# Performance work log

Measured on AMD Instinct MI355X. Metric: run time of the kernel, lower is better.

## Reference

```python
import jax, jax.numpy as jnp
import numpy as np

V, N, D, H, C = 3, 4096, 512, 128, 5  # views, nodes, in_dim, hidden, classes
NEG = -9.0e15   # mask value from original code (-9000000000000000.0)
NEG_SLOPE = 0.25


def _leaky(x, slope):
    return jnp.where(x >= 0, x, slope * x)


def setup_inputs() -> dict:
    key = jax.random.key(0)
    ks = jax.random.split(key, 24)
    g = lambda i, shape, s=0.05: (jax.random.normal(ks[i], shape, dtype=jnp.float32) * s)
    return {
        "data": jax.random.normal(ks[0], (V, N, D), dtype=jnp.float32),
        "adj": jax.random.randint(ks[1], (V, N, N), 0, 2, dtype=jnp.int32),
        "gac_w": g(2, (V, D, H)), "gac_b": g(3, (V, H)),
        "a1": g(4, (V, H)), "a2": g(5, (V, H)),
        "mlp_w": g(6, (V, D, H)), "mlp_b": g(7, (V, H)),
        "q_w": g(8, (V, H, H)), "q_b": g(9, (V, H)),
        "k_w": g(10, (V, H, H)), "k_b": g(11, (V, H)),
        "v_w": g(12, (V, H, H)), "v_b": g(13, (V, H)),
        "fc_w": g(14, (V, H, H)), "fc_b": g(15, (V, H)),
        "conf_w": g(16, (V, H, 1)), "conf_b": g(17, (V, 1)),
        "mm_w": g(18, (V * H, C)), "mm_b": g(19, (C,)),
    }


def reference(data, adj, gac_w, gac_b, a1, a2, mlp_w, mlp_b,
              q_w, q_b, k_w, k_b, v_w, v_b, fc_w, fc_b,
              conf_w, conf_b, mm_w, mm_b):
    # --- GraphAttentionConv (per view, vectorized over v) ---
    h = jnp.einsum('vnd,vdh->vnh', data, gac_w)               # spmm(input, W)
    e1 = jnp.einsum('vnh,vh->vn', h, a1)                      # h @ a1
    e2 = jnp.einsum('vnh,vh->vn', h, a2)                      # h @ a2
    e = _leaky(e1[:, :, None] + e2[:, None, :], NEG_SLOPE)    # [V,N,N] broadcast-add
    e = jnp.where(adj > 0, e, NEG)                            # mask by dense adjacency
    att = jax.nn.softmax(e, axis=-1)                          # row softmax
    feat = jnp.einsum('vnm,vmh->vnh', att, h) + gac_b[:, None, :]
    feat = _leaky(feat, NEG_SLOPE)                            # F.leaky_relu(GAC out, 0.25)
    # residual MLP branch
    feat = feat + jnp.einsum('vnd,vdh->vnh', data, mlp_w) + mlp_b[:, None, :]

    # --- StructureGuidedFeatureEnhancement (n_heads=1): per-node HxH attention ---
    Q = jnp.einsum('vnh,vho->vno', feat, q_w) + q_b[:, None, :]
    K = jnp.einsum('vnh,vho->vno', feat, k_w) + k_b[:, None, :]
    Vv = jnp.einsum('vnh,vho->vno', feat, v_w) + v_b[:, None, :]
    scale = jnp.sqrt(jnp.asarray(H, jnp.float32))
    A = Q[:, :, :, None] * K[:, :, None, :] / scale           # [V,N,H,H] outer product
    A = jax.nn.softmax(A, axis=-1)
    agg = jnp.einsum('vnio,vno->vni', A, Vv)                  # attention @ V
    agg = jnp.einsum('vnh,vho->vno', agg, fc_w) + fc_b[:, None, :]
    feat = jax.nn.relu(agg)

    # --- TCP confidence gating ---
    conf = jnp.einsum('vnh,vho->vno', feat, conf_w) + conf_b[:, None, :]  # [V,N,1]
    feat = feat * conf

    # --- concat views along feature dim, final classifier ---
    mm = jnp.transpose(feat, (1, 0, 2)).reshape(N, V * H)     # [N, V*H]
    return mm @ mm_w + mm_b                                   # MMlogit [N, C]
```

## Files before the change

kernel.cpp:

```cpp
#include <hip/hip_runtime.h>
#include <hip/hip_bf16.h>

#define V 3
#define N 4096
#define D 512
#define H 128
#define C 5
#define KS 2
#define LOG2E 1.4426950408889634f

typedef short short8 __attribute__((ext_vector_type(8)));
typedef float floatx4 __attribute__((ext_vector_type(4)));
typedef int   intx4  __attribute__((ext_vector_type(4)));

__device__ __forceinline__ unsigned short f2bf(float f){
  __hip_bfloat16 h = __float2bfloat16(f);
  return *reinterpret_cast<unsigned short*>(&h);
}
__device__ __forceinline__ unsigned int pk_bf16(float a, float b){
  unsigned int ua = __float_as_uint(a), ub = __float_as_uint(b);
  ua += 0x7FFFu + ((ua >> 16) & 1u);
  ub += 0x7FFFu + ((ub >> 16) & 1u);
  return (ua >> 16) | (ub & 0xFFFF0000u);
}

#define TN1 16
__global__ __launch_bounds__(256) void k1_gemm(
    const float* __restrict__ data,
    const float* __restrict__ gac_w,
    const float* __restrict__ mlp_w,
    const float* __restrict__ a1, const float* __restrict__ a2,
    unsigned short* __restrict__ hT, float* __restrict__ mlp_out,
    float* __restrict__ e1, float* __restrict__ e2)
{
  const int v = blockIdx.y;
  const int n0 = blockIdx.x * TN1;
  const int t = threadIdx.x;
  const int half = t >> 7, tt = t & 127;
  __shared__ float ds[D][20];
  __shared__ float epart[2][2][TN1];
  float* comb = &ds[0][0];
  const float* dp = data + ((size_t)v*N + n0)*D;
  for (int j = t; j < TN1*D; j += 256){
    int r = j >> 9, d = j & (D-1);
    ds[d][r] = dp[(size_t)r*D + d];
  }
  __syncthreads();
  float ag[TN1], am[TN1];
  #pragma unroll
  for (int r=0;r<TN1;r++){ ag[r]=0.f; am[r]=0.f; }
  const int d0 = half*256;
  const float* gw = gac_w + (size_t)v*D*H + tt;
  const float* mw = mlp_w + (size_t)v*D*H + tt;
  for (int d=d0; d<d0+256; d++){
    float wg = gw[(size_t)d*H];
    float wm = mw[(size_t)d*H];
    const float4* p = (const float4*)&ds[d][0];
    float4 x0=p[0], x1=p[1], x2=p[2], x3=p[3];
    float xv[16] = {x0.x,x0.y,x0.z,x0.w, x1.x,x1.y,x1.z,x1.w,
                    x2.x,x2.y,x2.z,x2.w, x3.x,x3.y,x3.z,x3.w};
    #pragma unroll
    for (int r=0;r<TN1;r++){
      ag[r] = fmaf(xv[r], wg, ag[r]);
      am[r] = fmaf(xv[r], wm, am[r]);
    }
  }
  __syncthreads();
  if (half == 1){
    #pragma unroll
    for (int r=0;r<TN1;r++){
      comb[r*H + tt]          = ag[r];
      comb[TN1*H + r*H + tt]  = am[r];
    }
  }
  __syncthreads();
  if (half == 0){
    float* mp = mlp_out + ((size_t)v*N + n0)*H + tt;
    unsigned short pk[TN1];
    const float a1v = a1[v*H + tt], a2v = a2[v*H + tt];
    #pragma unroll
    for (int r=0;r<TN1;r++){
      ag[r] += comb[r*H + tt];
      am[r] += comb[TN1*H + r*H + tt];
      mp[(size_t)r*H] = am[r];
      pk[r] = f2bf(ag[r]);
    }
    uint4* hp = (uint4*)(hT + ((size_t)v*H + tt)*N + n0);
    hp[0] = *(uint4*)&pk[0];
    hp[1] = *(uint4*)&pk[8];
    #pragma unroll
    for (int r=0;r<TN1;r++){
      float s1 = ag[r]*a1v, s2 = ag[r]*a2v;
      #pragma unroll
      for (int o=32;o>0;o>>=1){ s1 += __shfl_down(s1,o); s2 += __shfl_down(s2,o); }
      if ((tt&63)==0){ epart[0][tt>>6][r]=s1; epart[1][tt>>6][r]=s2; }
    }
  }
  __syncthreads();
  if (t < TN1)        e1[(size_t)v*N + n0 + t]       = LOG2E*(epart[0][0][t]    + epart[0][1][t]);
  else if (t < 2*TN1) e2[(size_t)v*N + n0 + (t-TN1)] = LOG2E*(epart[1][0][t-TN1]+ epart[1][1][t-TN1]);
}

#define KC2 256
__global__ __launch_bounds__(512, 8) void k2_attn(
    const unsigned short* __restrict__ hT, const int* __restrict__ adj,
    const float* __restrict__ e1g, const float* __restrict__ e2g,
    float* __restrict__ pacc, float* __restrict__ pdenG)
{
  const int v = blockIdx.z;
  const int ksid = blockIdx.y;
  const int n0 = blockIdx.x * 16;
  const int kbase = ksid * (N/KS);
  const int t = threadIdx.x;
  const int w = t >> 6, flane = t & 63;
  const int row = flane & 15, quad = flane >> 4;
  __shared__ __align__(16) unsigned short Afrag[2][8][64][8];
  __shared__ float pden_l[8][16];

  const intx4* ap4 = (const intx4*)(adj + ((size_t)v*N + n0 + row)*N
                                    + kbase + w*32 + quad*8);
  const float4* ep4 = (const float4*)(e2g + (size_t)v*N + kbase + w*32 + quad*8);
  const float e1r = e1g[(size_t)v*N + n0 + row];
  float psum = 0.f;

  const int col = w*16 + row;
  const unsigned short* bcol = hT + ((size_t)v*H + col)*N + kbase + quad*8;
  floatx4 acc = {0.f, 0.f, 0.f, 0.f};

  intx4  av0 = __builtin_nontemporal_load(ap4);
  intx4  av1 = __builtin_nontemporal_load(ap4 + 1);
  float4 ev0 = ep4[0];
  float4 ev1 = ep4[1];

  const int NCH = (N/KS)/KC2;
  #pragma unroll 1
  for (int c = 0; c < NCH; c++){
    {
      float ev[8] = {ev0.x,ev0.y,ev0.z,ev0.w, ev1.x,ev1.y,ev1.z,ev1.w};
      int   aa[8] = {av0.x,av0.y,av0.z,av0.w, av1.x,av1.y,av1.z,av1.w};
      float wv[8];
      #pragma unroll
      for (int j=0;j<8;j++){
        float y = e1r + ev[j];
        y = fmaxf(y, 0.25f*y);
        float e = exp2f(y);
        wv[j] = (aa[j] > 0) ? e : 0.f;
        psum += wv[j];
      }
      union { short8 s; unsigned int u[4]; } a8;
      #pragma unroll
      for (int j=0;j<4;j++) a8.u[j] = pk_bf16(wv[2*j], wv[2*j+1]);
      *(short8*)&Afrag[c&1][w][flane][0] = a8.s;
    }
    if (c+1 < NCH){
      av0 = __builtin_nontemporal_load(ap4 + (c+1)*64);
      av1 = __builtin_nontemporal_load(ap4 + (c+1)*64 + 1);
      ev0 = ep4[(c+1)*64];
      ev1 = ep4[(c+1)*64 + 1];
    }
    __syncthreads();
    const int m0 = c * KC2;
    #pragma unroll
    for (int ks=0; ks<8; ks++){
      short8 a8 = *(const short8*)&Afrag[c&1][ks][flane][0];
      short8 b8 = *(const short8*)(bcol + m0 + ks*32);
      acc = __builtin_amdgcn_mfma_f32_16x16x32_bf16(a8, b8, acc, 0, 0, 0);
    }
    __syncthreads();
  }
  psum += __shfl_down(psum, 32);
  psum += __shfl_down(psum, 16);
  if (flane < 16) pden_l[w][flane] = psum;
  __syncthreads();
  const size_t pb = (((size_t)v*KS + ksid)*(N/16) + blockIdx.x);
  float* pa = pacc + pb*(16*H);
  #pragma unroll
  for (int reg=0; reg<4; reg++){
    const int r = quad*4 + reg;
    pa[r*H + col] = acc[reg];
  }
  if (t < 16){
    float den = 0.f;
    #pragma unroll
    for (int k=0;k<8;k++) den += pden_l[k][t];
    pdenG[pb*16 + t] = den;
  }
}

__global__ __launch_bounds__(256) void k2_reduce(
    const float* __restrict__ pacc, const float* __restrict__ pdenG,
    const float* __restrict__ mlp_out,
    const float* __restrict__ gac_b, const float* __restrict__ mlp_b,
    float* __restrict__ feat)
{
  const int v = blockIdx.y;
  const int n0 = blockIdx.x * 16;
  const int t = threadIdx.x;
  const int col = t & 127, rh = t >> 7;
  const size_t pb0 = (((size_t)v*KS + 0)*(N/16) + blockIdx.x);
  const size_t pb1 = (((size_t)v*KS + 1)*(N/16) + blockIdx.x);
  const float* pa0 = pacc + pb0*(16*H);
  const float* pa1 = pacc + pb1*(16*H);
  const float gb = gac_b[v*H + col];
  const float mb = mlp_b[v*H + col];
  #pragma unroll
  for (int i=0;i<8;i++){
    const int r = rh*8 + i;
    float num = pa0[r*H + col] + pa1[r*H + col];
    float den = pdenG[pb0*16 + r] + pdenG[pb1*16 + r];
    float x = num/den + gb;
    x = (x >= 0.f) ? x : 0.25f*x;
    const size_t idx = ((size_t)v*N + n0 + r)*H + col;
    feat[idx] = x + mlp_out[idx] + mb;
  }
}

#define TN3 8
__global__ __launch_bounds__(128) void k3_sgfe(
    const float* __restrict__ feat,
    const float* __restrict__ qw, const float* __restrict__ qb,
    const float* __restrict__ kw, const float* __restrict__ kb,
    const float* __restrict__ vw, const float* __restrict__ vb,
    const float* __restrict__ fcw, const float* __restrict__ fcb,
    const float* __restrict__ confw, const float* __restrict__ confb,
    float* __restrict__ feat2)
{
  const int v = blockIdx.y;
  const int n0 = blockIdx.x * TN3;
  const int t = threadIdx.x;
  const int W = t >> 6, lane = t & 63;
  __shared__ float fsT[H][12];
  __shared__ float Qs[TN3][H];
  __shared__ float2 KVs[TN3][H];
  __shared__ float As2T[H][12];
  __shared__ float rbuf2[TN3][2];
  const float* fp = feat + ((size_t)v*N + n0)*H + t;
  #pragma unroll
  for (int r=0;r<TN3;r++) fsT[t][r] = fp[(size_t)r*H];
  __syncthreads();
  const float* qwp = qw + (size_t)v*H*H + t;
  const float* kwp = kw + (size_t)v*H*H + t;
  const float* vwp = vw + (size_t)v*H*H + t;
  float Qr[TN3], Kr[TN3], Vr[TN3];
  {
    const float qbv = qb[v*H+t], kbv = kb[v*H+t], vbv = vb[v*H+t];
    #pragma unroll
    for (int r=0;r<TN3;r++){ Qr[r]=qbv; Kr[r]=kbv; Vr[r]=vbv; }
  }
  for (int i=0;i<H;i++){
    float wq = qwp[(size_t)i*H];
    float wk = kwp[(size_t)i*H];
    float wv = vwp[(size_t)i*H];
    float4 f0 = *(const float4*)&fsT[i][0];
    float4 f1 = *(const float4*)&fsT[i][4];
    float fv[8] = {f0.x,f0.y,f0.z,f0.w, f1.x,f1.y,f1.z,f1.w};
    #pragma unroll
    for (int r=0;r<TN3;r++){
      Qr[r] = fmaf(fv[r], wq, Qr[r]);
      Kr[r] = fmaf(fv[r], wk, Kr[r]);
      Vr[r] = fmaf(fv[r], wv, Vr[r]);
    }
  }
  #pragma unroll
  for (int r=0;r<TN3;r++){
    Qs[r][t] = Qr[r];
    KVs[r][t] = make_float2(Kr[r], Vr[r]);
  }
  __syncthreads();
  const float invs = 0.08838834764831845f;
  #pragma unroll
  for (int p=0;p<4;p++){
    const int r = 2*p + W;
    const float qa = Qs[r][lane]   * invs;
    const float qb2 = Qs[r][lane+64] * invs;
    float sA=0.f, aA=0.f, sB=0.f, aB=0.f;
    const float4* kvp = (const float4*)&KVs[r][0];
    #pragma unroll 4
    for (int oo=0; oo<H/2; oo++){
      float4 kv2 = kvp[oo];
      float eA0 = __expf(qa*kv2.x);  sA += eA0; aA = fmaf(eA0, kv2.y, aA);
      float eA1 = __expf(qa*kv2.z);  sA += eA1; aA = fmaf(eA1, kv2.w, aA);
      float eB0 = __expf(qb2*kv2.x); sB += eB0; aB = fmaf(eB0, kv2.y, aB);
      float eB1 = __expf(qb2*kv2.z); sB += eB1; aB = fmaf(eB1, kv2.w, aB);
    }
    As2T[lane][r]    = aA/sA;
    As2T[lane+64][r] = aB/sB;
  }
  __syncthreads();
  const float* fcwp = fcw + (size_t)v*H*H + t;
  const float fcbv = fcb[v*H+t];
  float g[TN3];
  #pragma unroll
  for (int r=0;r<TN3;r++) g[r] = fcbv;
  for (int i=0;i<H;i++){
    float fw = fcwp[(size_t)i*H];
    float4 a0 = *(const float4*)&As2T[i][0];
    float4 a1v = *(const float4*)&As2T[i][4];
    g[0] = fmaf(a0.x, fw, g[0]);  g[1] = fmaf(a0.y, fw, g[1]);
    g[2] = fmaf(a0.z, fw, g[2]);  g[3] = fmaf(a0.w, fw, g[3]);
    g[4] = fmaf(a1v.x, fw, g[4]); g[5] = fmaf(a1v.y, fw, g[5]);
    g[6] = fmaf(a1v.z, fw, g[6]); g[7] = fmaf(a1v.w, fw, g[7]);
  }
  const float cwv = confw[v*H+t];
  const float cbv = confb[v];
  #pragma unroll
  for (int r=0;r<TN3;r++){
    g[r] = fmaxf(g[r], 0.f);
    float psm = g[r]*cwv;
    #pragma unroll
    for (int o=32;o>0;o>>=1) psm += __shfl_down(psm,o);
    if (lane==0) rbuf2[r][W] = psm;
  }
  __syncthreads();
  #pragma unroll
  for (int r=0;r<TN3;r++){
    const float conf = rbuf2[r][0] + rbuf2[r][1] + cbv;
    feat2[((size_t)v*N + n0 + r)*H + t] = g[r]*conf;
  }
}

__global__ __launch_bounds__(64) void k4_cls(
    const float* __restrict__ feat2,
    const float* __restrict__ mm_w, const float* __restrict__ mm_b,
    float* __restrict__ out)
{
  const int n = blockIdx.x, t = threadIdx.x;
  float a[C] = {0,0,0,0,0};
  for (int j=t; j<V*H; j+=64){
    int vv = j >> 7, hh = j & (H-1);
    float f = feat2[((size_t)vv*N + n)*H + hh];
    #pragma unroll
    for (int c=0;c<C;c++) a[c] = fmaf(f, mm_w[j*C+c], a[c]);
  }
  #pragma unroll
  for (int c=0;c<C;c++){
    #pragma unroll
    for (int o=32;o>0;o>>=1) a[c] += __shfl_down(a[c],o);
  }
  if (t==0){
    #pragma unroll
    for (int c=0;c<C;c++) out[(size_t)n*C+c] = a[c] + mm_b[c];
  }
}

extern "C" void kernel_launch(void* const* d_in, const int* in_sizes, int n_in,
                              void* d_out, int out_size, void* d_ws, size_t ws_size,
                              hipStream_t stream)
{
  (void)in_sizes; (void)n_in; (void)out_size; (void)ws_size;
  const float* data  = (const float*)d_in[0];
  const int*   adj   = (const int*)d_in[1];
  const float* gac_w = (const float*)d_in[2];
  const float* gac_b = (const float*)d_in[3];
  const float* a1    = (const float*)d_in[4];
  const float* a2    = (const float*)d_in[5];
  const float* mlp_w = (const float*)d_in[6];
  const float* mlp_b = (const float*)d_in[7];
  const float* q_w   = (const float*)d_in[8];
  const float* q_b   = (const float*)d_in[9];
  const float* k_w   = (const float*)d_in[10];
  const float* k_b   = (const float*)d_in[11];
  const float* v_w   = (const float*)d_in[12];
  const float* v_b   = (const float*)d_in[13];
  const float* fc_w  = (const float*)d_in[14];
  const float* fc_b  = (const float*)d_in[15];
  const float* cw    = (const float*)d_in[16];
  const float* cb    = (const float*)d_in[17];
  const float* mm_w  = (const float*)d_in[18];
  const float* mm_b  = (const float*)d_in[19];

  float* ws = (float*)d_ws;
  const size_t VNH = (size_t)V*N*H;
  float* mlp   = ws;
  float* feat  = ws + VNH;
  float* feat2 = ws + 2*VNH;
  float* e1    = ws + 3*VNH;
  float* e2    = e1 + (size_t)V*N;
  unsigned short* hT = (unsigned short*)(e2 + (size_t)V*N);
  float* pacc  = (float*)(hT + VNH);
  float* pden  = pacc + (size_t)V*KS*(N/16)*16*H;

  k1_gemm<<<dim3(N/TN1, V), 256, 0, stream>>>(data, gac_w, mlp_w, a1, a2,
                                              hT, mlp, e1, e2);
  k2_attn<<<dim3(N/16, KS, V), 512, 0, stream>>>(hT, adj, e1, e2, pacc, pden);
  k2_reduce<<<dim3(N/16, V), 256, 0, stream>>>(pacc, pden, mlp, gac_b, mlp_b, feat);
  k3_sgfe<<<dim3(N/TN3, V), 128, 0, stream>>>(feat, q_w, q_b, k_w, k_b, v_w, v_b,
                                              fc_w, fc_b, cw, cb, feat2);
  k4_cls<<<dim3(N),          64, 0, stream>>>(feat2, mm_w, mm_b, (float*)d_out);
}
```

Before: 525.1 us.

## Widen attention tile to 64 rows and split K four ways for hT reuse

The masked-softmax attention kernel now processes 64 query rows per block, with four row tiles sharing each hT B-fragment load across four MFMAs. Each wave handles two rows and one K-slice. The K dimension is split into 4 partitions instead of 2, and the reduce kernel is widened to sum four partials over 64-row tiles. This cuts repeated global reads of the bf16 hidden features, which were previously reloaded for every 16-row tile. In exchange it uses more registers and LDS per block and writes more partial-sum traffic to global memory.

```diff
diff --git a/kernel.cpp b/kernel.cpp
--- a/kernel.cpp
+++ b/kernel.cpp
@@ -6,7 +6,8 @@
 #define D 512
 #define H 128
 #define C 5
-#define KS 2
+#define KS 4
+#define M2 64
 #define LOG2E 1.4426950408889634f
 
 typedef short short8 __attribute__((ext_vector_type(8)));
@@ -101,116 +102,149 @@
   else if (t < 2*TN1) e2[(size_t)v*N + n0 + (t-TN1)] = LOG2E*(epart[1][0][t-TN1]+ epart[1][1][t-TN1]);
 }
 
-#define KC2 256
-__global__ __launch_bounds__(512, 8) void k2_attn(
+__global__ __launch_bounds__(512, 4) void k2_attn(
     const unsigned short* __restrict__ hT, const int* __restrict__ adj,
     const float* __restrict__ e1g, const float* __restrict__ e2g,
     float* __restrict__ pacc, float* __restrict__ pdenG)
 {
   const int v = blockIdx.z;
   const int ksid = blockIdx.y;
-  const int n0 = blockIdx.x * 16;
+  const int n0 = blockIdx.x * M2;
   const int kbase = ksid * (N/KS);
   const int t = threadIdx.x;
-  const int w = t >> 6, flane = t & 63;
-  const int row = flane & 15, quad = flane >> 4;
-  __shared__ __align__(16) unsigned short Afrag[2][8][64][8];
-  __shared__ float pden_l[8][16];
-
-  const intx4* ap4 = (const intx4*)(adj + ((size_t)v*N + n0 + row)*N
-                                    + kbase + w*32 + quad*8);
-  const float4* ep4 = (const float4*)(e2g + (size_t)v*N + kbase + w*32 + quad*8);
-  const float e1r = e1g[(size_t)v*N + n0 + row];
-  float psum = 0.f;
-
-  const int col = w*16 + row;
+  const int w = t >> 6, l = t & 63;
+  __shared__ __align__(16) unsigned short Afrag[2][4][4][64][8];
+  __shared__ float pden_sh[M2][4];
+
+  const int ksl  = w & 3;
+  const int quad = l >> 4;
+  const int rt0  = w >> 2;
+  const int row0 = rt0*16 + (l & 15);
+  const int row1 = row0 + 32;
+  const int koff = ksl*32 + quad*8;
+  const intx4* ap0 = (const intx4*)(adj + ((size_t)v*N + n0 + row0)*N + kbase + koff);
+  const intx4* ap1 = (const intx4*)(adj + ((size_t)v*N + n0 + row1)*N + kbase + koff);
+  const float4* ep = (const float4*)(e2g + (size_t)v*N + kbase + koff);
+  const float e1r0 = e1g[(size_t)v*N + n0 + row0];
+  const float e1r1 = e1g[(size_t)v*N + n0 + row1];
+  float psum0 = 0.f, psum1 = 0.f;
+
+  const int col = w*16 + (l & 15);
   const unsigned short* bcol = hT + ((size_t)v*H + col)*N + kbase + quad*8;
-  floatx4 acc = {0.f, 0.f, 0.f, 0.f};
-
-  intx4  av0 = __builtin_nontemporal_load(ap4);
-  intx4  av1 = __builtin_nontemporal_load(ap4 + 1);
-  float4 ev0 = ep4[0];
-  float4 ev1 = ep4[1];
-
-  const int NCH = (N/KS)/KC2;
+  floatx4 acc[4];
+  #pragma unroll
+  for (int rt=0;rt<4;rt++) acc[rt] = (floatx4){0.f,0.f,0.f,0.f};
+
+  intx4  a00 = __builtin_nontemporal_load(ap0);
+  intx4  a01 = __builtin_nontemporal_load(ap0 + 1);
+  intx4  a10 = __builtin_nontemporal_load(ap1);
+  intx4  a11 = __builtin_nontemporal_load(ap1 + 1);
+  float4 ev0 = ep[0];
+  float4 ev1 = ep[1];
+
+  const int NCH = (N/KS)/128;
   #pragma unroll 1
   for (int c = 0; c < NCH; c++){
+    const int buf = c & 1;
     {
       float ev[8] = {ev0.x,ev0.y,ev0.z,ev0.w, ev1.x,ev1.y,ev1.z,ev1.w};
-      int   aa[8] = {av0.x,av0.y,av0.z,av0.w, av1.x,av1.y,av1.z,av1.w};
-      float wv[8];
+      int   aa[8] = {a00.x,a00.y,a00.z,a00.w, a01.x,a01.y,a01.z,a01.w};
+      int   bb[8] = {a10.x,a10.y,a10.z,a10.w, a11.x,a11.y,a11.z,a11.w};
+      float wa[8], wb[8];
       #pragma unroll
       for (int j=0;j<8;j++){
-        float y = e1r + ev[j];
-        y = fmaxf(y, 0.25f*y);
-        float e = exp2f(y);
-        wv[j] = (aa[j] > 0) ? e : 0.f;
-        psum += wv[j];
+        float ya = e1r0 + ev[j];
+        ya = fmaxf(ya, 0.25f*ya);
+        float ea = exp2f(ya);
+        wa[j] = (aa[j] > 0) ? ea : 0.f;
+        psum0 += wa[j];
+        float yb = e1r1 + ev[j];
+        yb = fmaxf(yb, 0.25f*yb);
+        float eb = exp2f(yb);
+        wb[j] = (bb[j] > 0) ? eb : 0.f;
+        psum1 += wb[j];
       }
-      union { short8 s; unsigned int u[4]; } a8;
+      union { short8 s; unsigned int u[4]; } pa, pb;
       #pragma unroll
-      for (int j=0;j<4;j++) a8.u[j] = pk_bf16(wv[2*j], wv[2*j+1]);
-      *(short8*)&Afrag[c&1][w][flane][0] = a8.s;
+      for (int j=0;j<4;j++){
+        pa.u[j] = pk_bf16(wa[2*j], wa[2*j+1]);
+        pb.u[j] = pk_bf16(wb[2*j], wb[2*j+1]);
+      }
+      *(short8*)&Afrag[buf][rt0  ][ksl][l][0] = pa.s;
+      *(short8*)&Afrag[buf][rt0+2][ksl][l][0] = pb.s;
     }
     if (c+1 < NCH){
-      av0 = __builtin_nontemporal_load(ap4 + (c+1)*64);
-      av1 = __builtin_nontemporal_load(ap4 + (c+1)*64 + 1);
-      ev0 = ep4[(c+1)*64];
-      ev1 = ep4[(c+1)*64 + 1];
+      a00 = __builtin_nontemporal_load(ap0 + (c+1)*32);
+      a01 = __builtin_nontemporal_load(ap0 + (c+1)*32 + 1);
+      a10 = __builtin_nontemporal_load(ap1 + (c+1)*32);
+      a11 = __builtin_nontemporal_load(ap1 + (c+1)*32 + 1);
+      ev0 = ep[(c+1)*32];
+      ev1 = ep[(c+1)*32 + 1];
     }
     __syncthreads();
-    const int m0 = c * KC2;
-    #pragma unroll
-    for (int ks=0; ks<8; ks++){
-      short8 a8 = *(const short8*)&Afrag[c&1][ks][flane][0];
-      short8 b8 = *(const short8*)(bcol + m0 + ks*32);
-      acc = __builtin_amdgcn_mfma_f32_16x16x32_bf16(a8, b8, acc, 0, 0, 0);
+    #pragma unroll
+    for (int ks=0; ks<4; ks++){
+      short8 b8 = *(const short8*)(bcol + c*128 + ks*32);
+      #pragma unroll
+      for (int rt=0; rt<4; rt++){
+        short8 a8 = *(const short8*)&Afrag[buf][rt][ks][l][0];
+        acc[rt] = __builtin_amdgcn_mfma_f32_16x16x32_bf16(a8, b8, acc[rt], 0, 0, 0);
+      }
     }
     __syncthreads();
   }
-  psum += __shfl_down(psum, 32);
-  psum += __shfl_down(psum, 16);
-  if (flane < 16) pden_l[w][flane] = psum;
-  __syncthreads();
-  const size_t pb = (((size_t)v*KS + ksid)*(N/16) + blockIdx.x);
-  float* pa = pacc + pb*(16*H);
-  #pragma unroll
-  for (int reg=0; reg<4; reg++){
-    const int r = quad*4 + reg;
-    pa[r*H + col] = acc[reg];
-  }
-  if (t < 16){
-    float den = 0.f;
-    #pragma unroll
-    for (int k=0;k<8;k++) den += pden_l[k][t];
-    pdenG[pb*16 + t] = den;
-  }
-}
-
-__global__ __launch_bounds__(256) void k2_reduce(
+  psum0 += __shfl_xor(psum0, 16);
+  psum0 += __shfl_xor(psum0, 32);
+  psum1 += __shfl_xor(psum1, 16);
+  psum1 += __shfl_xor(psum1, 32);
+  if (l < 16){
+    pden_sh[row0][ksl] = psum0;
+    pden_sh[row1][ksl] = psum1;
+  }
+  __syncthreads();
+  const size_t pb = ((size_t)v*KS + ksid)*(N/M2) + blockIdx.x;
+  float* pa = pacc + pb*(M2*H);
+  #pragma unroll
+  for (int rt=0; rt<4; rt++){
+    #pragma unroll
+    for (int reg=0; reg<4; reg++){
+      const int row = rt*16 + quad*4 + reg;
+      pa[row*H + col] = acc[rt][reg];
+    }
+  }
+  if (t < M2){
+    float den = pden_sh[t][0] + pden_sh[t][1] + pden_sh[t][2] + pden_sh[t][3];
+    pdenG[pb*M2 + t] = den;
+  }
+}
+
+__global__ __launch_bounds__(512) void k2_reduce(
     const float* __restrict__ pacc, const float* __restrict__ pdenG,
     const float* __restrict__ mlp_out,
     const float* __restrict__ gac_b, const float* __restrict__ mlp_b,
     float* __restrict__ feat)
 {
   const int v = blockIdx.y;
-  const int n0 = blockIdx.x * 16;
+  const int n0 = blockIdx.x * M2;
   const int t = threadIdx.x;
-  const int col = t & 127, rh = t >> 7;
-  const size_t pb0 = (((size_t)v*KS + 0)*(N/16) + blockIdx.x);
-  const size_t pb1 = (((size_t)v*KS + 1)*(N/16) + blockIdx.x);
-  const float* pa0 = pacc + pb0*(16*H);
-  const float* pa1 = pacc + pb1*(16*H);
+  const int col = t & 127, rg = t >> 7;
+  size_t pb[KS];
+  #pragma unroll
+  for (int k=0;k<KS;k++) pb[k] = ((size_t)v*KS + k)*(N/M2) + blockIdx.x;
   const float gb = gac_b[v*H + col];
   const float mb = mlp_b[v*H + col];
   #pragma unroll
-  for (int i=0;i<8;i++){
-    const int r = rh*8 + i;
-    float num = pa0[r*H + col] + pa1[r*H + col];
-    float den = pdenG[pb0*16 + r] + pdenG[pb1*16 + r];
+  for (int i=0;i<16;i++){
+    const int row = rg*16 + i;
+    float num = 0.f, den = 0.f;
+    #pragma unroll
+    for (int k=0;k<KS;k++){
+      num += pacc[pb[k]*(M2*H) + row*H + col];
+      den += pdenG[pb[k]*M2 + row];
+    }
     float x = num/den + gb;
     x = (x >= 0.f) ? x : 0.25f*x;
-    const size_t idx = ((size_t)v*N + n0 + r)*H + col;
+    const size_t idx = ((size_t)v*N + n0 + row)*H + col;
     feat[idx] = x + mlp_out[idx] + mb;
   }
 }
@@ -378,12 +412,12 @@
   float* e2    = e1 + (size_t)V*N;
   unsigned short* hT = (unsigned short*)(e2 + (size_t)V*N);
   float* pacc  = (float*)(hT + VNH);
-  float* pden  = pacc + (size_t)V*KS*(N/16)*16*H;
+  float* pden  = pacc + (size_t)V*KS*(N/M2)*M2*H;
 
   k1_gemm<<<dim3(N/TN1, V), 256, 0, stream>>>(data, gac_w, mlp_w, a1, a2,
                                               hT, mlp, e1, e2);
-  k2_attn<<<dim3(N/16, KS, V), 512, 0, stream>>>(hT, adj, e1, e2, pacc, pden);
-  k2_reduce<<<dim3(N/16, V), 256, 0, stream>>>(pacc, pden, mlp, gac_b, mlp_b, feat);
+  k2_attn<<<dim3(N/M2, KS, V), 512, 0, stream>>>(hT, adj, e1, e2, pacc, pden);
+  k2_reduce<<<dim3(N/M2, V), 512, 0, stream>>>(pacc, pden, mlp, gac_b, mlp_b, feat);
   k3_sgfe<<<dim3(N/TN3, V), 128, 0, stream>>>(feat, q_w, q_b, k_w, k_b, v_w, v_b,
                                               fc_w, fc_b, cw, cb, feat2);
   k4_cls<<<dim3(N),          64, 0, stream>>>(feat2, mm_w, mm_b, (float*)d_out);
```

After: 475.3 us. -9.5%, faster.
